# Optimization experiments

Hardware: AMD Instinct MI355X
Metric: run time of the kernel (lower is better)

The kernel has to match this reference:

```python
import jax, jax.numpy as jnp
import numpy as np

EPS = 1e-6  # LayerNorm eps, added to std as in annotated-transformer LayerNorm


def _layernorm(x, gamma, beta):
    # torch-style: a_2*(x-mean)/(std+eps)+b_2, std is UNBIASED (ddof=1)
    mu = x.mean(axis=-1, keepdims=True)
    std = jnp.sqrt(x.var(axis=-1, ddof=1, keepdims=True))
    return gamma * (x - mu) / (std + EPS) + beta


def setup_inputs() -> dict:
    key = jax.random.key(0)
    ks = jax.random.split(key, 6)
    B, S, E, V = 32, 2048, 512, 32000
    return {
        "hidden_state": jax.random.normal(ks[0], (B, 1, E), jnp.float32),
        "output_sequence": jax.random.randint(ks[1], (B, S), 0, V),
        "emb_out": jax.random.normal(ks[2], (V, E), jnp.float32) * 0.02,
        "W_dec": jax.random.normal(ks[3], (E, E), jnp.float32) / np.sqrt(E),
        "b_dec": jnp.zeros((E,), jnp.float32),
        "gamma": jnp.ones((E,), jnp.float32),
        "beta": jnp.zeros((E,), jnp.float32),
        "W_voc": jax.random.normal(ks[4], (E, V), jnp.float32) / np.sqrt(E),
        "b_voc": jnp.zeros((V,), jnp.float32),
    }


def reference(hidden_state, output_sequence, emb_out, W_dec, b_dec, gamma, beta, W_voc, b_voc):
    E = emb_out.shape[1]
    # Embeddings: lookup scaled by sqrt(embed_dim)
    x = emb_out[output_sequence] * jnp.sqrt(jnp.asarray(E, emb_out.dtype))  # [B,S,E]

    def step(z, xt):  # z: [B,E], xt: [B,E]
        z = z + xt
        z = z + z @ W_dec + b_dec  # decoder_transfer with residual
        z = _layernorm(z, gamma, beta)
        return z, None

    z0 = jnp.zeros((x.shape[0], E), x.dtype)
    z, _ = jax.lax.scan(step, z0, jnp.swapaxes(x, 0, 1))  # scan over S
    z = z[:, None, :]  # [B,1,E]
    # VocabLogits: linear + log_softmax
    y = jax.nn.log_softmax(z @ W_voc + b_voc, axis=-1)  # [B,1,V]
    return z, y
```

## Files before the change

### kernel.cpp

```cpp
#include <hip/hip_runtime.h>
#include <math.h>

typedef float v4 __attribute__((ext_vector_type(4)));
typedef unsigned long long u64;

static constexpr int B_ = 32;
static constexpr int S_ = 2048;
static constexpr int E_ = 512;
static constexpr int V_ = 32000;
static constexpr float EPS_ = 1e-6f;
static constexpr int NH_ = 8;
static constexpr int CH_ = 64;

__global__ __launch_bounds__(1024) void scan8w(
    const int* __restrict__ seq,
    const float* __restrict__ emb,
    const float* __restrict__ Wdec,
    const float* __restrict__ bdec,
    const float* __restrict__ gamma,
    const float* __restrict__ beta,
    float* __restrict__ zout,
    u64* __restrict__ zpub)
{
    __shared__ __align__(16) float zs[E_];
    __shared__ __align__(16) float part[16][CH_];
    __shared__ float zmL[CH_];
    __shared__ float sred[16][2];
    __shared__ int   seq_l[S_];

    const int bid  = blockIdx.x;
    const int b    = bid & 31;
    const int h    = bid >> 5;
    const int c0   = h * CH_;
    const int tid  = threadIdx.x;
    const int wv   = tid >> 6;
    const int lane = tid & 63;
    const int cg   = lane & 15;
    const int sub  = lane >> 4;
    const int row0 = wv * 32 + sub * 8;

    v4 w[8];
    {
        const float* wp = Wdec + (size_t)row0 * E_ + c0 + 4 * cg;
        #pragma unroll
        for (int q = 0; q < 8; ++q) {
            const float* p = wp + (size_t)q * E_;
            asm volatile("global_load_dwordx4 %0, %1, off\n\ts_waitcnt vmcnt(0)"
                         : "=v"(w[q]) : "v"(p));
        }
    }

    const int* seqb = seq + (size_t)b * S_;
    for (int i = tid; i < S_; i += 1024) seq_l[i] = seqb[i];

    const float gmm = (tid < E_) ? gamma[tid] : 0.f;
    const float btt = (tid < E_) ? beta[tid] : 0.f;
    const float bdr = (tid < CH_) ? bdec[c0 + tid] : 0.f;
    const float sqrtE = sqrtf(512.0f);
    u64* zpb = zpub + (size_t)b * 2 * E_;

    __syncthreads();
    if (tid < E_) zs[tid] = emb[(size_t)seq_l[0] * E_ + tid] * sqrtE;
    __syncthreads();

    for (int t = 0; t < S_; ++t) {
        const int p = t & 1;
        const unsigned tag = (unsigned)(t + 1);

        const int tn = seq_l[(t + 1 < S_) ? t + 1 : t];
        float e = 0.f;
        if (tid < E_) e = emb[(size_t)tn * E_ + tid];

        const v4 za = *(const v4*)&zs[row0];
        const v4 zb = *(const v4*)&zs[row0 + 4];
        v4 acc = za.x * w[0];
        acc += za.y * w[1];
        acc += za.z * w[2];
        acc += za.w * w[3];
        acc += zb.x * w[4];
        acc += zb.y * w[5];
        acc += zb.z * w[6];
        acc += zb.w * w[7];
        acc.x += __shfl_down(acc.x, 16);
        acc.y += __shfl_down(acc.y, 16);
        acc.z += __shfl_down(acc.z, 16);
        acc.w += __shfl_down(acc.w, 16);
        acc.x += __shfl_down(acc.x, 32);
        acc.y += __shfl_down(acc.y, 32);
        acc.z += __shfl_down(acc.z, 32);
        acc.w += __shfl_down(acc.w, 32);
        if (lane < 16) *(v4*)&part[wv][4 * cg] = acc;
        __syncthreads();

        if (tid < CH_) {
            float sum = part[0][tid];
            #pragma unroll
            for (int k = 1; k < 16; ++k) sum += part[k][tid];
            const float zmid = zs[c0 + tid] + sum + bdr;
            zmL[tid] = zmid;
            union { float f; unsigned u; } cv; cv.f = zmid;
            const u64 pk = ((u64)tag << 32) | cv.u;
            __hip_atomic_store(&zpb[p * E_ + c0 + tid], pk,
                               __ATOMIC_RELAXED, __HIP_MEMORY_SCOPE_AGENT);
        }
        __syncthreads();

        float zmv = 0.f;
        if (tid < E_) {
            if ((tid >> 6) == h) {
                zmv = zmL[tid & 63];
            } else {
                u64 v;
                do {
                    v = __hip_atomic_load(&zpb[p * E_ + tid], __ATOMIC_RELAXED,
                                          __HIP_MEMORY_SCOPE_AGENT);
                } while ((unsigned)(v >> 32) != tag);
                union { unsigned u; float f; } cv; cv.u = (unsigned)v;
                zmv = cv.f;
            }
        }

        float s = zmv, q = zmv * zmv;
        #pragma unroll
        for (int off = 32; off > 0; off >>= 1) {
            s += __shfl_down(s, off);
            q += __shfl_down(q, off);
        }
        if (lane == 0) { sred[wv][0] = s; sred[wv][1] = q; }
        __syncthreads();

        float St = 0.f, Qt = 0.f;
        #pragma unroll
        for (int k = 0; k < 8; ++k) { St += sred[k][0]; Qt += sred[k][1]; }
        const float mu   = St * (1.0f / E_);
        const float var  = (Qt - St * mu) * (1.0f / (E_ - 1));
        const float invd = 1.0f / (sqrtf(var) + EPS_);
        const float zl   = gmm * (zmv - mu) * invd + btt;

        if (t == S_ - 1) {
            if (h == 0 && tid < E_) zout[(size_t)b * E_ + tid] = zl;
        } else if (tid < E_) {
            zs[tid] = fmaf(e, sqrtE, zl);
        }
        __syncthreads();
    }
}

__global__ __launch_bounds__(512) void logits_k(
    const float* __restrict__ zfin,
    const float* __restrict__ Wvoc,
    const float* __restrict__ bvoc,
    float* __restrict__ y)
{
    const int tid = threadIdx.x;
    const int col = blockIdx.x * 128 + (tid & 127);
    const int bg  = (tid >> 7) * 8;

    float acc[8] = {0.f, 0.f, 0.f, 0.f, 0.f, 0.f, 0.f, 0.f};
    const float* wp = Wvoc + col;
    const float* zp = zfin + (size_t)bg * E_;

    for (int k = 0; k < E_; k += 4) {
        const float w0 = wp[(size_t)(k + 0) * V_];
        const float w1 = wp[(size_t)(k + 1) * V_];
        const float w2 = wp[(size_t)(k + 2) * V_];
        const float w3 = wp[(size_t)(k + 3) * V_];
        #pragma unroll
        for (int g = 0; g < 8; ++g) {
            acc[g] = fmaf(zp[g * E_ + k + 0], w0, acc[g]);
            acc[g] = fmaf(zp[g * E_ + k + 1], w1, acc[g]);
            acc[g] = fmaf(zp[g * E_ + k + 2], w2, acc[g]);
            acc[g] = fmaf(zp[g * E_ + k + 3], w3, acc[g]);
        }
    }
    const float bv = bvoc[col];
    #pragma unroll
    for (int g = 0; g < 8; ++g)
        y[(size_t)(bg + g) * V_ + col] = acc[g] + bv;
}

__global__ __launch_bounds__(1024) void lse_k(
    const float* __restrict__ y, float* __restrict__ corr)
{
    __shared__ float redm[16], redl[16];
    const int b = blockIdx.x;
    const int tid = threadIdx.x;
    const float* row = y + (size_t)b * V_;

    float m = -3.0e38f, l = 0.f;
    for (int v = tid; v < V_; v += 1024) {
        const float x = row[v];
        const float nm = fmaxf(m, x);
        l = l * __expf(m - nm) + __expf(x - nm);
        m = nm;
    }
    #pragma unroll
    for (int off = 32; off > 0; off >>= 1) {
        const float om = __shfl_down(m, off);
        const float ol = __shfl_down(l, off);
        const float nm = fmaxf(m, om);
        l = l * __expf(m - nm) + ol * __expf(om - nm);
        m = nm;
    }
    const int lane = tid & 63, wvv = tid >> 6;
    if (lane == 0) { redm[wvv] = m; redl[wvv] = l; }
    __syncthreads();
    if (tid == 0) {
        float M = redm[0], L = redl[0];
        for (int k = 1; k < 16; ++k) {
            const float nm = fmaxf(M, redm[k]);
            L = L * __expf(M - nm) + redl[k] * __expf(redm[k] - nm);
            M = nm;
        }
        corr[b] = M + logf(L);
    }
}

__global__ __launch_bounds__(256) void fix_k(
    float* __restrict__ y, const float* __restrict__ corr)
{
    const int idx = blockIdx.x * 256 + threadIdx.x;
    const size_t o = (size_t)idx * 4;
    const int b = (int)(o / V_);
    const float cr = corr[b];
    v4 v = *(v4*)(y + o);
    v = v - cr;
    *(v4*)(y + o) = v;
}

extern "C" void kernel_launch(void* const* d_in, const int* in_sizes, int n_in,
                              void* d_out, int out_size, void* d_ws, size_t ws_size,
                              hipStream_t stream)
{
    (void)in_sizes; (void)n_in; (void)out_size; (void)ws_size;
    const int*   seq  = (const int*)  d_in[1];
    const float* emb  = (const float*)d_in[2];
    const float* Wdec = (const float*)d_in[3];
    const float* bdec = (const float*)d_in[4];
    const float* gam  = (const float*)d_in[5];
    const float* bet  = (const float*)d_in[6];
    const float* Wvoc = (const float*)d_in[7];
    const float* bvoc = (const float*)d_in[8];

    float* out  = (float*)d_out;
    float* zout = out;
    float* y    = out + B_ * E_;

    u64*   zpub = (u64*)d_ws;
    float* corr = (float*)((char*)d_ws + (size_t)B_ * 2 * E_ * sizeof(u64));

    hipMemsetAsync(zpub, 0, (size_t)B_ * 2 * E_ * sizeof(u64), stream);

    hipLaunchKernelGGL(scan8w, dim3(B_ * NH_), dim3(1024), 0, stream,
                       seq, emb, Wdec, bdec, gam, bet, zout, zpub);
    hipLaunchKernelGGL(logits_k, dim3(V_ / 128), dim3(512), 0, stream,
                       zout, Wvoc, bvoc, y);
    hipLaunchKernelGGL(lse_k, dim3(B_), dim3(1024), 0, stream, y, corr);
    hipLaunchKernelGGL(fix_k, dim3(1000), dim3(256), 0, stream, y, corr);
}
```

Measured before the change: 4.354 ms.

## Restructure scan step: per-wave column ownership, exchange partial LayerNorm stats across blocks

Each wave now owns 4 output columns and reduces the full 512-row dot product with an xor butterfly, so the shared-memory partial-sum stage and one block barrier go away. Each block publishes its partial sum and sum of squares to global memory, and wave 0 polls all eight blocks' stats to compute the mean and inverse std. Meanwhile waves 8-15 gather the full mid vector into shared memory. This removes a barrier per step and overlaps stat exchange with the vector gather, at the cost of extra global spin polling and more shuffle work per wave.

```diff
diff --git a/kernel.cpp b/kernel.cpp
--- a/kernel.cpp
+++ b/kernel.cpp
@@ -23,9 +23,9 @@
     u64* __restrict__ zpub)
 {
     __shared__ __align__(16) float zs[E_];
-    __shared__ __align__(16) float part[16][CH_];
-    __shared__ float zmL[CH_];
+    __shared__ __align__(16) float zmbuf[E_];
     __shared__ float sred[16][2];
+    __shared__ float munv[2];
     __shared__ int   seq_l[S_];
 
     const int bid  = blockIdx.x;
@@ -35,13 +35,10 @@
     const int tid  = threadIdx.x;
     const int wv   = tid >> 6;
     const int lane = tid & 63;
-    const int cg   = lane & 15;
-    const int sub  = lane >> 4;
-    const int row0 = wv * 32 + sub * 8;
 
     v4 w[8];
     {
-        const float* wp = Wdec + (size_t)row0 * E_ + c0 + 4 * cg;
+        const float* wp = Wdec + (size_t)(8 * lane) * E_ + c0 + 4 * wv;
         #pragma unroll
         for (int q = 0; q < 8; ++q) {
             const float* p = wp + (size_t)q * E_;
@@ -55,9 +52,10 @@
 
     const float gmm = (tid < E_) ? gamma[tid] : 0.f;
     const float btt = (tid < E_) ? beta[tid] : 0.f;
-    const float bdr = (tid < CH_) ? bdec[c0 + tid] : 0.f;
+    const v4 bd4 = *(const v4*)(bdec + c0 + 4 * wv);
     const float sqrtE = sqrtf(512.0f);
     u64* zpb = zpub + (size_t)b * 2 * E_;
+    u64* zst = zpub + (size_t)B_ * 2 * E_ + (size_t)b * 32;
 
     __syncthreads();
     if (tid < E_) zs[tid] = emb[(size_t)seq_l[0] * E_ + tid] * sqrtE;
@@ -71,8 +69,8 @@
         float e = 0.f;
         if (tid < E_) e = emb[(size_t)tn * E_ + tid];
 
-        const v4 za = *(const v4*)&zs[row0];
-        const v4 zb = *(const v4*)&zs[row0 + 4];
+        const v4 za = *(const v4*)&zs[8 * lane];
+        const v4 zb = *(const v4*)&zs[8 * lane + 4];
         v4 acc = za.x * w[0];
         acc += za.y * w[1];
         acc += za.z * w[2];
@@ -81,66 +79,88 @@
         acc += zb.y * w[5];
         acc += zb.z * w[6];
         acc += zb.w * w[7];
-        acc.x += __shfl_down(acc.x, 16);
-        acc.y += __shfl_down(acc.y, 16);
-        acc.z += __shfl_down(acc.z, 16);
-        acc.w += __shfl_down(acc.w, 16);
-        acc.x += __shfl_down(acc.x, 32);
-        acc.y += __shfl_down(acc.y, 32);
-        acc.z += __shfl_down(acc.z, 32);
-        acc.w += __shfl_down(acc.w, 32);
-        if (lane < 16) *(v4*)&part[wv][4 * cg] = acc;
+        #pragma unroll
+        for (int m = 1; m < 64; m <<= 1) {
+            acc.x += __shfl_xor(acc.x, m);
+            acc.y += __shfl_xor(acc.y, m);
+            acc.z += __shfl_xor(acc.z, m);
+            acc.w += __shfl_xor(acc.w, m);
+        }
+        const v4 zp4 = *(const v4*)&zs[c0 + 4 * wv];
+        const v4 zm4 = acc + zp4 + bd4;
+
+        if (lane < 4) {
+            const float zv = (lane == 0) ? zm4.x : (lane == 1) ? zm4.y
+                           : (lane == 2) ? zm4.z : zm4.w;
+            union { float f; unsigned u; } cv; cv.f = zv;
+            __hip_atomic_store(&zpb[p * E_ + c0 + 4 * wv + lane],
+                               ((u64)tag << 32) | cv.u,
+                               __ATOMIC_RELAXED, __HIP_MEMORY_SCOPE_AGENT);
+        }
+        if (lane == 0) {
+            sred[wv][0] = zm4.x + zm4.y + zm4.z + zm4.w;
+            sred[wv][1] = zm4.x * zm4.x + zm4.y * zm4.y
+                        + zm4.z * zm4.z + zm4.w * zm4.w;
+        }
         __syncthreads();
 
-        if (tid < CH_) {
-            float sum = part[0][tid];
-            #pragma unroll
-            for (int k = 1; k < 16; ++k) sum += part[k][tid];
-            const float zmid = zs[c0 + tid] + sum + bdr;
-            zmL[tid] = zmid;
-            union { float f; unsigned u; } cv; cv.f = zmid;
-            const u64 pk = ((u64)tag << 32) | cv.u;
-            __hip_atomic_store(&zpb[p * E_ + c0 + tid], pk,
-                               __ATOMIC_RELAXED, __HIP_MEMORY_SCOPE_AGENT);
+        if (wv == 0) {
+            float s = 0.f, q = 0.f;
+            if (lane < 16) { s = sred[lane][0]; q = sred[lane][1]; }
+            s += __shfl_down(s, 8);  q += __shfl_down(q, 8);
+            s += __shfl_down(s, 4);  q += __shfl_down(q, 4);
+            s += __shfl_down(s, 2);  q += __shfl_down(q, 2);
+            s += __shfl_down(s, 1);  q += __shfl_down(q, 1);
+            if (lane == 0) {
+                union { float f; unsigned u; } c1, c2; c1.f = s; c2.f = q;
+                __hip_atomic_store(&zst[p * 16 + 0 + h], ((u64)tag << 32) | c1.u,
+                                   __ATOMIC_RELAXED, __HIP_MEMORY_SCOPE_AGENT);
+                __hip_atomic_store(&zst[p * 16 + 8 + h], ((u64)tag << 32) | c2.u,
+                                   __ATOMIC_RELAXED, __HIP_MEMORY_SCOPE_AGENT);
+            }
+            float v = 0.f;
+            if (lane < 16) {
+                const u64* addr = &zst[p * 16 + (lane & 8) + (lane & 7)];
+                u64 x;
+                do {
+                    x = __hip_atomic_load(addr, __ATOMIC_RELAXED,
+                                          __HIP_MEMORY_SCOPE_AGENT);
+                } while ((unsigned)(x >> 32) != tag);
+                union { unsigned u; float f; } cv; cv.u = (unsigned)x;
+                v = cv.f;
+            }
+            v += __shfl_xor(v, 1);
+            v += __shfl_xor(v, 2);
+            v += __shfl_xor(v, 4);
+            const float qt = __shfl(v, 8);
+            if (lane == 0) {
+                const float St  = v;
+                const float mu  = St * (1.0f / E_);
+                const float var = (qt - St * mu) * (1.0f / (E_ - 1));
+                munv[0] = mu;
+                munv[1] = 1.0f / (sqrtf(var) + EPS_);
+            }
+        } else if (wv >= 8) {
+            const int i = tid - 512;
+            const u64* addr = &zpb[p * E_ + i];
+            u64 x;
+            do {
+                x = __hip_atomic_load(addr, __ATOMIC_RELAXED,
+                                      __HIP_MEMORY_SCOPE_AGENT);
+            } while ((unsigned)(x >> 32) != tag);
+            union { unsigned u; float f; } cv; cv.u = (unsigned)x;
+            zmbuf[i] = cv.f;
         }
         __syncthreads();
 
-        float zmv = 0.f;
         if (tid < E_) {
-            if ((tid >> 6) == h) {
-                zmv = zmL[tid & 63];
+            const float mu = munv[0], invd = munv[1];
+            const float zl = gmm * (zmbuf[tid] - mu) * invd + btt;
+            if (t == S_ - 1) {
+                if (h == 0) zout[(size_t)b * E_ + tid] = zl;
             } else {
-                u64 v;
-                do {
-                    v = __hip_atomic_load(&zpb[p * E_ + tid], __ATOMIC_RELAXED,
-                                          __HIP_MEMORY_SCOPE_AGENT);
-                } while ((unsigned)(v >> 32) != tag);
-                union { unsigned u; float f; } cv; cv.u = (unsigned)v;
-                zmv = cv.f;
-            }
-        }
-
-        float s = zmv, q = zmv * zmv;
-        #pragma unroll
-        for (int off = 32; off > 0; off >>= 1) {
-            s += __shfl_down(s, off);
-            q += __shfl_down(q, off);
-        }
-        if (lane == 0) { sred[wv][0] = s; sred[wv][1] = q; }
-        __syncthreads();
-
-        float St = 0.f, Qt = 0.f;
-        #pragma unroll
-        for (int k = 0; k < 8; ++k) { St += sred[k][0]; Qt += sred[k][1]; }
-        const float mu   = St * (1.0f / E_);
-        const float var  = (Qt - St * mu) * (1.0f / (E_ - 1));
-        const float invd = 1.0f / (sqrtf(var) + EPS_);
-        const float zl   = gmm * (zmv - mu) * invd + btt;
-
-        if (t == S_ - 1) {
-            if (h == 0 && tid < E_) zout[(size_t)b * E_ + tid] = zl;
-        } else if (tid < E_) {
-            zs[tid] = fmaf(e, sqrtE, zl);
+                zs[tid] = fmaf(e, sqrtE, zl);
+            }
         }
         __syncthreads();
     }
@@ -246,10 +266,11 @@
     float* zout = out;
     float* y    = out + B_ * E_;
 
+    const size_t exch_u64 = (size_t)B_ * 2 * E_ + (size_t)B_ * 32;
     u64*   zpub = (u64*)d_ws;
-    float* corr = (float*)((char*)d_ws + (size_t)B_ * 2 * E_ * sizeof(u64));
-
-    hipMemsetAsync(zpub, 0, (size_t)B_ * 2 * E_ * sizeof(u64), stream);
+    float* corr = (float*)((char*)d_ws + exch_u64 * sizeof(u64));
+
+    hipMemsetAsync(zpub, 0, exch_u64 * sizeof(u64), stream);
 
     hipLaunchKernelGGL(scan8w, dim3(B_ * NH_), dim3(1024), 0, stream,
                        seq, emb, Wdec, bdec, gam, bet, zout, zpub);
```

Result: slower. 5.373 ms (+23.4%).

## Exchange per-slice LayerNorm partial sums and poll remote slices in spare waves

Applied to the files above, without the earlier changes.

Each of the 8 head blocks per batch row now computes its own sum and sum-of-squares over its 64-column slice and publishes them with tagged atomics. A dedicated wave polls for the other blocks' statistics, and waves 9-15 poll for the remote z values and write them to shared memory. This removes one block-wide reduction and its __syncthreads from each scan step, and moves the spin-waiting off the LayerNorm waves. The cost is extra atomic traffic and a larger exchange buffer, and the variance is now combined from partial sums in a different order.

```diff
diff --git a/kernel.cpp b/kernel.cpp
--- a/kernel.cpp
+++ b/kernel.cpp
@@ -24,8 +24,8 @@
 {
     __shared__ __align__(16) float zs[E_];
     __shared__ __align__(16) float part[16][CH_];
-    __shared__ float zmL[CH_];
-    __shared__ float sred[16][2];
+    __shared__ __align__(16) float zmbuf[E_];
+    __shared__ float sst[NH_][2];
     __shared__ int   seq_l[S_];
 
     const int bid  = blockIdx.x;
@@ -58,6 +58,10 @@
     const float bdr = (tid < CH_) ? bdec[c0 + tid] : 0.f;
     const float sqrtE = sqrtf(512.0f);
     u64* zpb = zpub + (size_t)b * 2 * E_;
+    u64* zst = zpub + (size_t)B_ * 2 * E_ + (size_t)b * 32;
+
+    int pe = 0;
+    if (wv >= 9) { const int j = tid - 576; pe = j + ((j >= c0) ? CH_ : 0); }
 
     __syncthreads();
     if (tid < E_) zs[tid] = emb[(size_t)seq_l[0] * E_ + tid] * sqrtE;
@@ -97,50 +101,67 @@
             #pragma unroll
             for (int k = 1; k < 16; ++k) sum += part[k][tid];
             const float zmid = zs[c0 + tid] + sum + bdr;
-            zmL[tid] = zmid;
             union { float f; unsigned u; } cv; cv.f = zmid;
-            const u64 pk = ((u64)tag << 32) | cv.u;
-            __hip_atomic_store(&zpb[p * E_ + c0 + tid], pk,
+            __hip_atomic_store(&zpb[p * E_ + c0 + tid],
+                               ((u64)tag << 32) | cv.u,
                                __ATOMIC_RELAXED, __HIP_MEMORY_SCOPE_AGENT);
+            zmbuf[c0 + tid] = zmid;
+            float s = zmid, q2 = zmid * zmid;
+            #pragma unroll
+            for (int m = 1; m < 64; m <<= 1) {
+                s  += __shfl_xor(s, m);
+                q2 += __shfl_xor(q2, m);
+            }
+            if (tid == 0) {
+                union { float f; unsigned u; } c1, c2; c1.f = s; c2.f = q2;
+                __hip_atomic_store(&zst[p * 16 + 0 + h], ((u64)tag << 32) | c1.u,
+                                   __ATOMIC_RELAXED, __HIP_MEMORY_SCOPE_AGENT);
+                __hip_atomic_store(&zst[p * 16 + 8 + h], ((u64)tag << 32) | c2.u,
+                                   __ATOMIC_RELAXED, __HIP_MEMORY_SCOPE_AGENT);
+                sst[h][0] = s; sst[h][1] = q2;
+            }
+        } else if (wv == 8) {
+            if (lane < 16) {
+                const int i = lane & 7, k = lane >> 3;
+                if (i != h) {
+                    const u64* ap = &zst[p * 16 + k * 8 + i];
+                    u64 v;
+                    do {
+                        v = __hip_atomic_load(ap, __ATOMIC_RELAXED,
+                                              __HIP_MEMORY_SCOPE_AGENT);
+                    } while ((unsigned)(v >> 32) != tag);
+                    union { unsigned u; float f; } cv; cv.u = (unsigned)v;
+                    sst[i][k] = cv.f;
+                }
+            }
+        } else if (wv >= 9) {
+            const u64* ap = &zpb[p * E_ + pe];
+            u64 v;
+            do {
+                v = __hip_atomic_load(ap, __ATOMIC_RELAXED,
+                                      __HIP_MEMORY_SCOPE_AGENT);
+            } while ((unsigned)(v >> 32) != tag);
+            union { unsigned u; float f; } cv; cv.u = (unsigned)v;
+            zmbuf[pe] = cv.f;
         }
         __syncthreads();
 
-        float zmv = 0.f;
         if (tid < E_) {
-            if ((tid >> 6) == h) {
-                zmv = zmL[tid & 63];
+            const float St =
+                ((sst[0][0] + sst[1][0]) + (sst[2][0] + sst[3][0]))
+              + ((sst[4][0] + sst[5][0]) + (sst[6][0] + sst[7][0]));
+            const float Qt =
+                ((sst[0][1] + sst[1][1]) + (sst[2][1] + sst[3][1]))
+              + ((sst[4][1] + sst[5][1]) + (sst[6][1] + sst[7][1]));
+            const float mu   = St * (1.0f / E_);
+            const float var  = (Qt - St * mu) * (1.0f / (E_ - 1));
+            const float invd = 1.0f / (sqrtf(var) + EPS_);
+            const float zl   = gmm * (zmbuf[tid] - mu) * invd + btt;
+            if (t == S_ - 1) {
+                if (h == 0) zout[(size_t)b * E_ + tid] = zl;
             } else {
-                u64 v;
-                do {
-                    v = __hip_atomic_load(&zpb[p * E_ + tid], __ATOMIC_RELAXED,
-                                          __HIP_MEMORY_SCOPE_AGENT);
-                } while ((unsigned)(v >> 32) != tag);
-                union { unsigned u; float f; } cv; cv.u = (unsigned)v;
-                zmv = cv.f;
-            }
-        }
-
-        float s = zmv, q = zmv * zmv;
-        #pragma unroll
-        for (int off = 32; off > 0; off >>= 1) {
-            s += __shfl_down(s, off);
-            q += __shfl_down(q, off);
-        }
-        if (lane == 0) { sred[wv][0] = s; sred[wv][1] = q; }
-        __syncthreads();
-
-        float St = 0.f, Qt = 0.f;
-        #pragma unroll
-        for (int k = 0; k < 8; ++k) { St += sred[k][0]; Qt += sred[k][1]; }
-        const float mu   = St * (1.0f / E_);
-        const float var  = (Qt - St * mu) * (1.0f / (E_ - 1));
-        const float invd = 1.0f / (sqrtf(var) + EPS_);
-        const float zl   = gmm * (zmv - mu) * invd + btt;
-
-        if (t == S_ - 1) {
-            if (h == 0 && tid < E_) zout[(size_t)b * E_ + tid] = zl;
-        } else if (tid < E_) {
-            zs[tid] = fmaf(e, sqrtE, zl);
+                zs[tid] = fmaf(e, sqrtE, zl);
+            }
         }
         __syncthreads();
     }
@@ -246,10 +267,11 @@
     float* zout = out;
     float* y    = out + B_ * E_;
 
+    const size_t exch_u64 = (size_t)B_ * 2 * E_ + (size_t)B_ * 32;
     u64*   zpub = (u64*)d_ws;
-    float* corr = (float*)((char*)d_ws + (size_t)B_ * 2 * E_ * sizeof(u64));
-
-    hipMemsetAsync(zpub, 0, (size_t)B_ * 2 * E_ * sizeof(u64), stream);
+    float* corr = (float*)((char*)d_ws + exch_u64 * sizeof(u64));
+
+    hipMemsetAsync(zpub, 0, exch_u64 * sizeof(u64), stream);
 
     hipLaunchKernelGGL(scan8w, dim3(B_ * NH_), dim3(1024), 0, stream,
                        seq, emb, Wdec, bdec, gam, bet, zout, zpub);
```

New measurement: 4.552 ms. 4.6% more time.
